# Kernel optimization log

Hardware: AMD Instinct MI355X
Metric: run time of the kernel (lower is better)

Reference implementation:

```python
import jax, jax.numpy as jnp
import numpy as np

NEG_INF = -1e6

def setup_inputs() -> dict:
    key = jax.random.key(0)
    ks = jax.random.split(key, 7)
    B, Q, K, D, H = 16, 64, 1024, 256, 128
    return {
        "queries": jax.random.normal(ks[0], (B, Q, D), dtype=jnp.float32),
        "keys": jax.random.normal(ks[1], (B, K, D), dtype=jnp.float32),
        "values": jax.random.normal(ks[2], (B, K, D), dtype=jnp.float32),
        "valid_lens": jax.random.randint(ks[3], (B,), 1, K + 1, dtype=jnp.int32),
        "W_q": jax.random.normal(ks[4], (D, H), dtype=jnp.float32) * (1.0 / np.sqrt(D)),
        "W_k": jax.random.normal(ks[5], (D, H), dtype=jnp.float32) * (1.0 / np.sqrt(D)),
        "w_v": jax.random.normal(ks[6], (H,), dtype=jnp.float32) * (1.0 / np.sqrt(H)),
    }

def reference(queries, keys, values, valid_lens, W_q, W_k, w_v):
    # project: [B,Q,H], [B,K,H]
    q = jnp.einsum('bqd,dh->bqh', queries, W_q)
    k = jnp.einsum('bkd,dh->bkh', keys, W_k)
    # broadcast add -> tanh -> score: [B,Q,K]
    features = jnp.tanh(q[:, :, None, :] + k[:, None, :, :])  # [B,Q,K,H]
    scores = jnp.einsum('bqkh,h->bqk', features, w_v)
    # masked softmax over key axis (valid_lens per batch)
    K_len = keys.shape[1]
    mask = jnp.arange(K_len)[None, None, :] < valid_lens[:, None, None]  # [B,1,K]
    scores = jnp.where(mask, scores, NEG_INF)
    attn = jax.nn.softmax(scores, axis=-1)
    # weighted sum of values: [B,Q,Dv]  (dropout p=0 -> identity)
    return jnp.einsum('bqk,bkd->bqd', attn, values)
```

## Files before the change

kernel.cpp:

```cpp
#include <hip/hip_runtime.h>

#define DDIM 256
#define HDIM 128
#define KLEN 1024
#define SCL 2.8853900817779268f

__global__ __launch_bounds__(256) void proj_kernel(
    const float* __restrict__ queries, const float* __restrict__ keys,
    const float* __restrict__ W_q, const float* __restrict__ W_k,
    float* __restrict__ Eq, float* __restrict__ Ek)
{
    __shared__ union {
        float a[64 * 64];
        float t[32][68];
    } sm;

    const int tid  = threadIdx.x;
    const int lane = tid & 63;
    const int wav  = tid >> 6;

    int blk = blockIdx.x;
    bool iskey; int b = 0, kc0 = 0, hb, row0;
    const float* in; const float* W;
    if (blk < 1024) {
        iskey = true;
        int xcd = blk & 7, s = blk >> 3;
        b = ((s >> 6) << 3) | xcd;
        int r6 = s & 63;
        kc0 = (r6 >> 2) << 6;
        hb  = (r6 & 3) << 5;
        row0 = b * KLEN + kc0;
        in = keys; W = W_k;
    } else {
        iskey = false;
        int qrb = blk - 1024;
        row0 = (qrb >> 2) << 6;
        hb   = (qrb & 3) << 5;
        in = queries; W = W_q;
    }

    const int hg8 = __builtin_amdgcn_readfirstlane(wav << 3);
    const float* Wu = W + hb + hg8;

    const int srow = tid >> 4;
    const int sgd  = tid & 15;
    const float* gsrc = in + (size_t)(row0 + srow) * DDIM + (sgd << 2);

    float4 pf0 = *(const float4*)(gsrc);
    float4 pf1 = *(const float4*)(gsrc + 16 * DDIM);
    float4 pf2 = *(const float4*)(gsrc + 32 * DDIM);
    float4 pf3 = *(const float4*)(gsrc + 48 * DDIM);

    float acc[8];
    #pragma unroll
    for (int c = 0; c < 8; c++) acc[c] = 0.f;

    const int w0 = (srow)      * 64 + ((sgd ^ ((srow)      & 7)) << 2);
    const int w1 = (srow + 16) * 64 + ((sgd ^ ((srow + 16) & 7)) << 2);
    const int w2 = (srow + 32) * 64 + ((sgd ^ ((srow + 32) & 7)) << 2);
    const int w3 = (srow + 48) * 64 + ((sgd ^ ((srow + 48) & 7)) << 2);

    for (int dt0 = 0; dt0 < DDIM; dt0 += 64) {
        *(float4*)(sm.a + w0) = pf0;
        *(float4*)(sm.a + w1) = pf1;
        *(float4*)(sm.a + w2) = pf2;
        *(float4*)(sm.a + w3) = pf3;
        __syncthreads();
        if (dt0 < DDIM - 64) {
            const float* g2 = gsrc + dt0 + 64;
            pf0 = *(const float4*)(g2);
            pf1 = *(const float4*)(g2 + 16 * DDIM);
            pf2 = *(const float4*)(g2 + 32 * DDIM);
            pf3 = *(const float4*)(g2 + 48 * DDIM);
        }
        const float* arow = sm.a + lane * 64;
        const int lx = lane & 7;
        #pragma unroll
        for (int d4 = 0; d4 < 64; d4 += 4) {
            float4 a = *(const float4*)(arow + ((((d4 >> 2)) ^ lx) << 2));
            const float* wr = Wu + (size_t)(dt0 + d4) * HDIM;
            #pragma unroll
            for (int c = 0; c < 8; c++) acc[c] = fmaf(a.x, wr[c],            acc[c]);
            #pragma unroll
            for (int c = 0; c < 8; c++) acc[c] = fmaf(a.y, wr[HDIM + c],     acc[c]);
            #pragma unroll
            for (int c = 0; c < 8; c++) acc[c] = fmaf(a.z, wr[2 * HDIM + c], acc[c]);
            #pragma unroll
            for (int c = 0; c < 8; c++) acc[c] = fmaf(a.w, wr[3 * HDIM + c], acc[c]);
        }
        __syncthreads();
    }

    float e[8];
    #pragma unroll
    for (int c = 0; c < 8; c++) e[c] = __builtin_amdgcn_exp2f(SCL * acc[c]);

    if (!iskey) {
        float* dst = Eq + (size_t)(row0 + lane) * HDIM + hb + hg8;
        *(float4*)(dst)     = make_float4(e[0], e[1], e[2], e[3]);
        *(float4*)(dst + 4) = make_float4(e[4], e[5], e[6], e[7]);
    } else {
        #pragma unroll
        for (int c = 0; c < 8; c++) sm.t[(wav << 3) + c][lane] = e[c];
        __syncthreads();
        float* dstb = Ek + (size_t)b * HDIM * KLEN + (size_t)hb * KLEN + kc0;
        #pragma unroll
        for (int i = 0; i < 2; i++) {
            int g = tid + (i << 8);
            int h = g >> 4, k4 = (g & 15) << 2;
            float4 o = *(const float4*)(&sm.t[h][k4]);
            *(float4*)(dstb + (size_t)h * KLEN + k4) = o;
        }
    }
}

__global__ __launch_bounds__(256) void score_av_kernel(
    const float* __restrict__ Eq, const float* __restrict__ Ek,
    const float* __restrict__ w_v, const int* __restrict__ valid_lens,
    const float* __restrict__ values,
    float* __restrict__ part, float* __restrict__ Tp)
{
    __shared__ union {
        struct {
            float4 eqw[4][HDIM];
            float  el[128][8];
        } p;
        float4 slab[4][8][64];
    } sm;
    __shared__ float tslab[4][8];

    const int tid = threadIdx.x;
    const int lane = tid & 63, wav = tid >> 6;
    int blk = blockIdx.x;
    int xcd = blk & 7, s = blk >> 3;
    int b = ((s >> 6) << 3) | xcd;
    int r = s & 63;
    int qt = r >> 3, kq = r & 7;
    int bq0 = b * 64 + qt * 8;
    int k0g = kq << 7;
    int vlen = valid_lens[b];

    if (k0g >= vlen) {
        float4 z = make_float4(0.f, 0.f, 0.f, 0.f);
        #pragma unroll
        for (int e = 0; e < 2; e++) {
            int slot = (tid << 1) | e;
            int q = slot >> 6, d4 = slot & 63;
            *(float4*)(part + ((size_t)kq * 1024 + bq0 + q) * DDIM + (d4 << 2)) = z;
        }
        if (tid < 8) Tp[(size_t)kq * 1024 + bq0 + tid] = 0.f;
        return;
    }

    #pragma unroll
    for (int i = 0; i < 2; i++) {
        int slot = tid + (i << 8);
        int w = slot >> 7, h = slot & 127;
        sm.p.eqw[w][h] = make_float4(
            Eq[(size_t)(bq0 + 2 * w) * HDIM + h],
            Eq[(size_t)(bq0 + 2 * w + 1) * HDIM + h],
            -2.0f * w_v[h], 0.f);
    }
    __syncthreads();

    const int kl = lane << 1;
    const float* ekp = Ek + (size_t)b * HDIM * KLEN + k0g + kl;
    float2 buf[8];
    #pragma unroll
    for (int j = 0; j < 8; j++)
        buf[j] = *(const float2*)(ekp + (size_t)j * KLEN);

    float2 acc0 = make_float2(0.f, 0.f), acc1 = make_float2(0.f, 0.f);
    for (int h0 = 0; h0 < HDIM; h0 += 8) {
        float2 nxt[8];
        if (h0 < HDIM - 8) {
            #pragma unroll
            for (int j = 0; j < 8; j++)
                nxt[j] = *(const float2*)(ekp + (size_t)(h0 + 8 + j) * KLEN);
        }
        #pragma unroll
        for (int j = 0; j < 8; j++) {
            float4 e = sm.p.eqw[wav][h0 + j];
            float2 ek = buf[j];
            acc0.x = fmaf(e.z, __builtin_amdgcn_rcpf(fmaf(e.x, ek.x, 1.f)), acc0.x);
            acc0.y = fmaf(e.z, __builtin_amdgcn_rcpf(fmaf(e.x, ek.y, 1.f)), acc0.y);
            acc1.x = fmaf(e.z, __builtin_amdgcn_rcpf(fmaf(e.y, ek.x, 1.f)), acc1.x);
            acc1.y = fmaf(e.z, __builtin_amdgcn_rcpf(fmaf(e.y, ek.y, 1.f)), acc1.y);
        }
        #pragma unroll
        for (int j = 0; j < 8; j++) buf[j] = nxt[j];
    }

    {
        int kg = k0g + kl;
        float e00 = (kg     < vlen) ? __expf(acc0.x) : 0.f;
        float e01 = (kg + 1 < vlen) ? __expf(acc0.y) : 0.f;
        float e10 = (kg     < vlen) ? __expf(acc1.x) : 0.f;
        float e11 = (kg + 1 < vlen) ? __expf(acc1.y) : 0.f;
        *(float2*)(&sm.p.el[kl][2 * wav])     = make_float2(e00, e10);
        *(float2*)(&sm.p.el[kl + 1][2 * wav]) = make_float2(e01, e11);
    }
    __syncthreads();

    int kw = wav << 5;
    int kg0 = k0g + kw;
    int cnt = vlen - kg0; cnt = cnt < 0 ? 0 : (cnt > 32 ? 32 : cnt);
    int cnt4 = (cnt + 3) & ~3;
    const float* vb = values + ((size_t)b * KLEN + kg0) * DDIM + (lane << 2);

    float4 acc[8];
    float acct[8];
    #pragma unroll
    for (int q = 0; q < 8; q++) { acc[q] = make_float4(0.f, 0.f, 0.f, 0.f); acct[q] = 0.f; }

    for (int k = 0; k < cnt4; k += 4) {
        #pragma unroll
        for (int j = 0; j < 4; j++) {
            float4 v  = *(const float4*)(vb + (size_t)(k + j) * DDIM);
            float4 p0 = *(const float4*)(&sm.p.el[kw + k + j][0]);
            float4 p1 = *(const float4*)(&sm.p.el[kw + k + j][4]);
            float pq[8] = {p0.x, p0.y, p0.z, p0.w, p1.x, p1.y, p1.z, p1.w};
            #pragma unroll
            for (int q = 0; q < 8; q++) {
                acc[q].x = fmaf(pq[q], v.x, acc[q].x);
                acc[q].y = fmaf(pq[q], v.y, acc[q].y);
                acc[q].z = fmaf(pq[q], v.z, acc[q].z);
                acc[q].w = fmaf(pq[q], v.w, acc[q].w);
                acct[q] += pq[q];
            }
        }
    }

    __syncthreads();
    #pragma unroll
    for (int q = 0; q < 8; q++) sm.slab[wav][q][lane] = acc[q];
    if (lane == 0) {
        #pragma unroll
        for (int q = 0; q < 8; q++) tslab[wav][q] = acct[q];
    }
    __syncthreads();
    #pragma unroll
    for (int e = 0; e < 2; e++) {
        int slot = (tid << 1) | e;
        int q = slot >> 6, d4 = slot & 63;
        float4 a = sm.slab[0][q][d4];
        #pragma unroll
        for (int g = 1; g < 4; g++) {
            float4 t = sm.slab[g][q][d4];
            a.x += t.x; a.y += t.y; a.z += t.z; a.w += t.w;
        }
        *(float4*)(part + ((size_t)kq * 1024 + bq0 + q) * DDIM + (d4 << 2)) = a;
    }
    if (tid < 8) {
        float t = tslab[0][tid] + tslab[1][tid] + tslab[2][tid] + tslab[3][tid];
        Tp[(size_t)kq * 1024 + bq0 + tid] = t;
    }
}

__global__ __launch_bounds__(256) void combine_kernel(
    const float* __restrict__ part, const float* __restrict__ Tp,
    float* __restrict__ out)
{
    int i = blockIdx.x * 256 + threadIdx.x;
    int row = i >> 6;
    const float4* p4 = (const float4*)part;
    float t = 0.f;
    #pragma unroll
    for (int j = 0; j < 8; j++) t += Tp[(size_t)j * 1024 + row];
    float inv = 1.0f / t;
    float4 a = p4[i];
    #pragma unroll
    for (int j = 1; j < 8; j++) {
        float4 v = p4[(size_t)j * 65536 + i];
        a.x += v.x; a.y += v.y; a.z += v.z; a.w += v.w;
    }
    a.x *= inv; a.y *= inv; a.z *= inv; a.w *= inv;
    ((float4*)out)[i] = a;
}

extern "C" void kernel_launch(void* const* d_in, const int* in_sizes, int n_in,
                              void* d_out, int out_size, void* d_ws, size_t ws_size,
                              hipStream_t stream) {
    const float* queries    = (const float*)d_in[0];
    const float* keys       = (const float*)d_in[1];
    const float* values     = (const float*)d_in[2];
    const int*   valid_lens = (const int*)d_in[3];
    const float* W_q        = (const float*)d_in[4];
    const float* W_k        = (const float*)d_in[5];
    const float* w_v        = (const float*)d_in[6];

    float* Eq   = (float*)d_ws;
    float* Ek   = Eq + 131072;
    float* part = Ek + 2097152;
    float* Tp   = part + 2097152;

    proj_kernel<<<1088, 256, 0, stream>>>(queries, keys, W_q, W_k, Eq, Ek);
    score_av_kernel<<<1024, 256, 0, stream>>>(Eq, Ek, w_v, valid_lens, values, part, Tp);
    combine_kernel<<<256, 256, 0, stream>>>(part, Tp, (float*)d_out);
}
```

Measured before the change: 137.7 us.

## Split key axis into 16 chunks of 64 and cut score kernel LDS usage

Result: slower. 161.5 us (+17.3%).

```diff
diff --git a/kernel.cpp b/kernel.cpp
--- a/kernel.cpp
+++ b/kernel.cpp
@@ -114,30 +114,25 @@
     }
 }
 
-__global__ __launch_bounds__(256) void score_av_kernel(
+__global__ __launch_bounds__(256, 8) void score_av_kernel(
     const float* __restrict__ Eq, const float* __restrict__ Ek,
     const float* __restrict__ w_v, const int* __restrict__ valid_lens,
     const float* __restrict__ values,
     float* __restrict__ part, float* __restrict__ Tp)
 {
-    __shared__ union {
-        struct {
-            float4 eqw[4][HDIM];
-            float  el[128][8];
-        } p;
-        float4 slab[4][8][64];
-    } sm;
-    __shared__ float tslab[4][8];
+    __shared__ float el[64][12];
+    __shared__ float accbuf[8][256];
+    __shared__ float tacc[8];
 
     const int tid = threadIdx.x;
     const int lane = tid & 63, wav = tid >> 6;
     int blk = blockIdx.x;
     int xcd = blk & 7, s = blk >> 3;
-    int b = ((s >> 6) << 3) | xcd;
-    int r = s & 63;
-    int qt = r >> 3, kq = r & 7;
+    int b = ((s >> 7) << 3) | xcd;
+    int r = s & 127;
+    int qt = r >> 4, ks = r & 15;
     int bq0 = b * 64 + qt * 8;
-    int k0g = kq << 7;
+    int k0g = ks << 6;
     int vlen = valid_lens[b];
 
     if (k0g >= vlen) {
@@ -146,67 +141,57 @@
         for (int e = 0; e < 2; e++) {
             int slot = (tid << 1) | e;
             int q = slot >> 6, d4 = slot & 63;
-            *(float4*)(part + ((size_t)kq * 1024 + bq0 + q) * DDIM + (d4 << 2)) = z;
-        }
-        if (tid < 8) Tp[(size_t)kq * 1024 + bq0 + tid] = 0.f;
+            *(float4*)(part + ((size_t)ks * 1024 + bq0 + q) * DDIM + (d4 << 2)) = z;
+        }
+        if (tid < 8) Tp[(size_t)ks * 1024 + bq0 + tid] = 0.f;
         return;
     }
 
-    #pragma unroll
-    for (int i = 0; i < 2; i++) {
-        int slot = tid + (i << 8);
-        int w = slot >> 7, h = slot & 127;
-        sm.p.eqw[w][h] = make_float4(
-            Eq[(size_t)(bq0 + 2 * w) * HDIM + h],
-            Eq[(size_t)(bq0 + 2 * w + 1) * HDIM + h],
-            -2.0f * w_v[h], 0.f);
+    const int q0 = wav << 1;
+    const float* ekp = Ek + (size_t)b * HDIM * KLEN + k0g + lane;
+    const float* eqa = Eq + (size_t)(bq0 + q0) * HDIM;
+    const float* eqb = eqa + HDIM;
+
+    float ekc[4], ekn[4], eac[4], ean[4], ebc[4], ebn[4], wvc[4], wvn[4];
+    #pragma unroll
+    for (int j = 0; j < 4; j++) ekc[j] = ekp[(size_t)j * KLEN];
+    *(float4*)&eac[0] = *(const float4*)(eqa);
+    *(float4*)&ebc[0] = *(const float4*)(eqb);
+    *(float4*)&wvc[0] = *(const float4*)(w_v);
+
+    float acc0 = 0.f, acc1 = 0.f;
+    for (int h0 = 0; h0 < HDIM; h0 += 4) {
+        if (h0 < HDIM - 4) {
+            #pragma unroll
+            for (int j = 0; j < 4; j++) ekn[j] = ekp[(size_t)(h0 + 4 + j) * KLEN];
+            *(float4*)&ean[0] = *(const float4*)(eqa + h0 + 4);
+            *(float4*)&ebn[0] = *(const float4*)(eqb + h0 + 4);
+            *(float4*)&wvn[0] = *(const float4*)(w_v + h0 + 4);
+        }
+        #pragma unroll
+        for (int j = 0; j < 4; j++) {
+            float w2 = -2.0f * wvc[j];
+            acc0 = fmaf(w2, __builtin_amdgcn_rcpf(fmaf(eac[j], ekc[j], 1.f)), acc0);
+            acc1 = fmaf(w2, __builtin_amdgcn_rcpf(fmaf(ebc[j], ekc[j], 1.f)), acc1);
+        }
+        #pragma unroll
+        for (int j = 0; j < 4; j++) {
+            ekc[j] = ekn[j]; eac[j] = ean[j]; ebc[j] = ebn[j]; wvc[j] = wvn[j];
+        }
+    }
+
+    {
+        int kg = k0g + lane;
+        float e0 = (kg < vlen) ? __expf(acc0) : 0.f;
+        float e1 = (kg < vlen) ? __expf(acc1) : 0.f;
+        *(float2*)(&el[lane][q0]) = make_float2(e0, e1);
     }
     __syncthreads();
 
-    const int kl = lane << 1;
-    const float* ekp = Ek + (size_t)b * HDIM * KLEN + k0g + kl;
-    float2 buf[8];
-    #pragma unroll
-    for (int j = 0; j < 8; j++)
-        buf[j] = *(const float2*)(ekp + (size_t)j * KLEN);
-
-    float2 acc0 = make_float2(0.f, 0.f), acc1 = make_float2(0.f, 0.f);
-    for (int h0 = 0; h0 < HDIM; h0 += 8) {
-        float2 nxt[8];
-        if (h0 < HDIM - 8) {
-            #pragma unroll
-            for (int j = 0; j < 8; j++)
-                nxt[j] = *(const float2*)(ekp + (size_t)(h0 + 8 + j) * KLEN);
-        }
-        #pragma unroll
-        for (int j = 0; j < 8; j++) {
-            float4 e = sm.p.eqw[wav][h0 + j];
-            float2 ek = buf[j];
-            acc0.x = fmaf(e.z, __builtin_amdgcn_rcpf(fmaf(e.x, ek.x, 1.f)), acc0.x);
-            acc0.y = fmaf(e.z, __builtin_amdgcn_rcpf(fmaf(e.x, ek.y, 1.f)), acc0.y);
-            acc1.x = fmaf(e.z, __builtin_amdgcn_rcpf(fmaf(e.y, ek.x, 1.f)), acc1.x);
-            acc1.y = fmaf(e.z, __builtin_amdgcn_rcpf(fmaf(e.y, ek.y, 1.f)), acc1.y);
-        }
-        #pragma unroll
-        for (int j = 0; j < 8; j++) buf[j] = nxt[j];
-    }
-
-    {
-        int kg = k0g + kl;
-        float e00 = (kg     < vlen) ? __expf(acc0.x) : 0.f;
-        float e01 = (kg + 1 < vlen) ? __expf(acc0.y) : 0.f;
-        float e10 = (kg     < vlen) ? __expf(acc1.x) : 0.f;
-        float e11 = (kg + 1 < vlen) ? __expf(acc1.y) : 0.f;
-        *(float2*)(&sm.p.el[kl][2 * wav])     = make_float2(e00, e10);
-        *(float2*)(&sm.p.el[kl + 1][2 * wav]) = make_float2(e01, e11);
-    }
-    __syncthreads();
-
-    int kw = wav << 5;
-    int kg0 = k0g + kw;
-    int cnt = vlen - kg0; cnt = cnt < 0 ? 0 : (cnt > 32 ? 32 : cnt);
+    int kw = wav << 4;
+    int cnt = vlen - (k0g + kw); cnt = cnt < 0 ? 0 : (cnt > 16 ? 16 : cnt);
     int cnt4 = (cnt + 3) & ~3;
-    const float* vb = values + ((size_t)b * KLEN + kg0) * DDIM + (lane << 2);
+    const float* vb = values + ((size_t)b * KLEN + k0g + kw) * DDIM + (lane << 2);
 
     float4 acc[8];
     float acct[8];
@@ -217,8 +202,8 @@
         #pragma unroll
         for (int j = 0; j < 4; j++) {
             float4 v  = *(const float4*)(vb + (size_t)(k + j) * DDIM);
-            float4 p0 = *(const float4*)(&sm.p.el[kw + k + j][0]);
-            float4 p1 = *(const float4*)(&sm.p.el[kw + k + j][4]);
+            float4 p0 = *(const float4*)(&el[kw + k + j][0]);
+            float4 p1 = *(const float4*)(&el[kw + k + j][4]);
             float pq[8] = {p0.x, p0.y, p0.z, p0.w, p1.x, p1.y, p1.z, p1.w};
             #pragma unroll
             for (int q = 0; q < 8; q++) {
@@ -232,29 +217,41 @@
     }
 
     __syncthreads();
-    #pragma unroll
-    for (int q = 0; q < 8; q++) sm.slab[wav][q][lane] = acc[q];
-    if (lane == 0) {
-        #pragma unroll
-        for (int q = 0; q < 8; q++) tslab[wav][q] = acct[q];
+    if (wav == 0) {
+        #pragma unroll
+        for (int q = 0; q < 8; q++)
+            *(float4*)(&accbuf[q][lane << 2]) = acc[q];
+        if (lane == 0) {
+            #pragma unroll
+            for (int q = 0; q < 8; q++) tacc[q] = acct[q];
+        }
     }
     __syncthreads();
+    #pragma unroll
+    for (int w = 1; w < 4; w++) {
+        if (wav == w) {
+            #pragma unroll
+            for (int q = 0; q < 8; q++) {
+                float4 t = *(const float4*)(&accbuf[q][lane << 2]);
+                t.x += acc[q].x; t.y += acc[q].y; t.z += acc[q].z; t.w += acc[q].w;
+                *(float4*)(&accbuf[q][lane << 2]) = t;
+            }
+            if (lane == 0) {
+                #pragma unroll
+                for (int q = 0; q < 8; q++) tacc[q] += acct[q];
+            }
+        }
+        __syncthreads();
+    }
+
     #pragma unroll
     for (int e = 0; e < 2; e++) {
         int slot = (tid << 1) | e;
         int q = slot >> 6, d4 = slot & 63;
-        float4 a = sm.slab[0][q][d4];
-        #pragma unroll
-        for (int g = 1; g < 4; g++) {
-            float4 t = sm.slab[g][q][d4];
-            a.x += t.x; a.y += t.y; a.z += t.z; a.w += t.w;
-        }
-        *(float4*)(part + ((size_t)kq * 1024 + bq0 + q) * DDIM + (d4 << 2)) = a;
-    }
-    if (tid < 8) {
-        float t = tslab[0][tid] + tslab[1][tid] + tslab[2][tid] + tslab[3][tid];
-        Tp[(size_t)kq * 1024 + bq0 + tid] = t;
-    }
+        *(float4*)(part + ((size_t)ks * 1024 + bq0 + q) * DDIM + (d4 << 2)) =
+            *(const float4*)(&accbuf[q][d4 << 2]);
+    }
+    if (tid < 8) Tp[(size_t)ks * 1024 + bq0 + tid] = tacc[tid];
 }
 
 __global__ __launch_bounds__(256) void combine_kernel(
@@ -266,11 +263,11 @@
     const float4* p4 = (const float4*)part;
     float t = 0.f;
     #pragma unroll
-    for (int j = 0; j < 8; j++) t += Tp[(size_t)j * 1024 + row];
+    for (int j = 0; j < 16; j++) t += Tp[(size_t)j * 1024 + row];
     float inv = 1.0f / t;
     float4 a = p4[i];
     #pragma unroll
-    for (int j = 1; j < 8; j++) {
+    for (int j = 1; j < 16; j++) {
         float4 v = p4[(size_t)j * 65536 + i];
         a.x += v.x; a.y += v.y; a.z += v.z; a.w += v.w;
     }
@@ -292,9 +289,9 @@
     float* Eq   = (float*)d_ws;
     float* Ek   = Eq + 131072;
     float* part = Ek + 2097152;
-    float* Tp   = part + 2097152;
+    float* Tp   = part + 4194304;
 
     proj_kernel<<<1088, 256, 0, stream>>>(queries, keys, W_q, W_k, Eq, Ek);
-    score_av_kernel<<<1024, 256, 0, stream>>>(Eq, Ek, w_v, valid_lens, values, part, Tp);
+    score_av_kernel<<<2048, 256, 0, stream>>>(Eq, Ek, w_v, valid_lens, values, part, Tp);
     combine_kernel<<<256, 256, 0, stream>>>(part, Tp, (float*)d_out);
 }
```
